# Kernel optimization log

Measured on AMD Instinct MI355X. Metric: run time of the kernel, lower is better.

Reference implementation:

```python
import jax, jax.numpy as jnp
import numpy as np

GROUP_SIZE = 128
TOP_K = 2
ZERO_POINT = 8  # Marlin symmetric zero point: w = scale * (q - 8)


def _dequant_int4(q, scales, group_size):
    # q: [E, N, K] int values in [0,15]; scales: [E, N, K//group_size]
    s = jnp.repeat(scales, group_size, axis=-1)  # [E, N, K]
    return (q.astype(jnp.float32) - float(ZERO_POINT)) * s


def setup_inputs() -> dict:
    key = jax.random.key(0)
    k1, k2, k3, k4, k5, k6 = jax.random.split(key, 6)
    B, S, H, I, E = 2, 1024, 2048, 1408, 8
    router_logits = jax.random.normal(k1, (B, S, E), dtype=jnp.float32)
    hidden_states = jax.random.normal(k2, (B, S, H), dtype=jnp.float32)
    fc_gate_up_qweights = jax.random.randint(k3, (E, 2 * I, H), 0, 16, dtype=jnp.int32)
    fc_gate_up_scales = jax.random.uniform(k4, (E, 2 * I, H // GROUP_SIZE), dtype=jnp.float32) * 0.02
    fc_down_qweights = jax.random.randint(k5, (E, H, I), 0, 16, dtype=jnp.int32)
    fc_down_scales = jax.random.uniform(k6, (E, H, I // GROUP_SIZE), dtype=jnp.float32) * 0.02
    return {
        "router_logits": router_logits,
        "hidden_states": hidden_states,
        "fc_gate_up_qweights": fc_gate_up_qweights,
        "fc_gate_up_scales": fc_gate_up_scales,
        "fc_down_qweights": fc_down_qweights,
        "fc_down_scales": fc_down_scales,
    }


def reference(router_logits, hidden_states, fc_gate_up_qweights, fc_gate_up_scales,
              fc_down_qweights, fc_down_scales):
    B, S, H = hidden_states.shape
    E = router_logits.shape[-1]
    T = B * S
    x = hidden_states.reshape(T, H)
    logits = router_logits.reshape(T, E)

    # top-k routing with softmax over selected logits
    top_vals, top_idx = jax.lax.top_k(logits, TOP_K)          # [T, k]
    top_w = jax.nn.softmax(top_vals, axis=-1)                 # [T, k]
    route_w = jnp.zeros((T, E), x.dtype).at[jnp.arange(T)[:, None], top_idx].set(top_w)  # [T, E]

    # dequantize int4 weights: scale * (q - 8), per-group along K
    w_gate_up = _dequant_int4(fc_gate_up_qweights, fc_gate_up_scales, GROUP_SIZE)  # [E, 2I, H]
    w_down = _dequant_int4(fc_down_qweights, fc_down_scales, GROUP_SIZE)          # [E, H, I]

    # grouped GEMM (dense over experts, masked by routing weights)
    gu = jnp.einsum('th,enh->ten', x, w_gate_up)              # [T, E, 2I]
    gate, up = jnp.split(gu, 2, axis=-1)
    act = jax.nn.silu(gate) * up                              # SwiGLU, [T, E, I]
    out = jnp.einsum('tei,ehi,te->th', act, w_down, route_w)  # [T, H]
    return out.reshape(B, S, H)
```

## Files before the change

kernel.cpp:

```cpp
#include <hip/hip_runtime.h>
#include <hip/hip_fp16.h>

#define T_TOKENS 2048
#define H_DIM    2048
#define I_DIM    1408
#define E_NUM    8

typedef _Float16 f16;
typedef __attribute__((ext_vector_type(8))) _Float16 f16x8;
typedef __attribute__((ext_vector_type(4))) float    floatx4;
typedef __attribute__((ext_vector_type(4))) unsigned uintx4;

static const size_t OFF_COUNTS = 0;
static const size_t OFF_LISTS  = 256;
static const size_t OFF_WLISTS = OFF_LISTS + (size_t)T_TOKENS * E_NUM * 4;
static const size_t OFF_XB     = 131328;
static const size_t OFF_ACT    = OFF_XB + (size_t)T_TOKENS * H_DIM * 2;
static const size_t OFF_GUPK   = OFF_ACT + (size_t)2 * T_TOKENS * I_DIM * 2;
static const size_t OFF_DNPK   = OFF_GUPK + (size_t)E_NUM * 22 * 32 * 128 * 8 * 4;
static const size_t OFF_TMP    = OFF_DNPK + (size_t)E_NUM * 16 * 22 * 128 * 8 * 4;


__global__ __launch_bounds__(256) void pack_gu_kernel(const int* __restrict__ q,
                                                      unsigned* __restrict__ out)
{
    const int b = blockIdx.x;
    const int g = threadIdx.x;
    const int4* qp = reinterpret_cast<const int4*>(q + (size_t)b * H_DIM) + g * 2;
    int4 a = qp[0], c = qp[1];
    unsigned d = (unsigned)(a.x & 15)        | ((unsigned)(a.z & 15) << 4)  |
                 ((unsigned)(c.x & 15) << 8) | ((unsigned)(c.z & 15) << 12) |
                 ((unsigned)(a.y & 15) << 16)| ((unsigned)(a.w & 15) << 20) |
                 ((unsigned)(c.y & 15) << 24)| ((unsigned)(c.w & 15) << 28);
    const int e = b / 2816;
    const int grow = b - e * 2816;
    const int is_up = grow >= I_DIM;
    const int icol  = grow - (is_up ? I_DIM : 0);
    const int nt    = icol >> 6;
    const int r     = ((((icol >> 4) & 3) * 2 + is_up) * 16) + (icol & 15);
    const int kt    = g >> 3, gg = g & 7;
    out[((((size_t)e * 22 + nt) * 32 + kt) * 128 + r) * 8 + (gg ^ (r & 7))] = d;
}

__global__ __launch_bounds__(256) void pack_dn_kernel(const int* __restrict__ q,
                                                      unsigned* __restrict__ out)
{
    const int b = blockIdx.x;
    const int t = threadIdx.x;
    if (t >= 176) return;
    const int4* qp = reinterpret_cast<const int4*>(q + (size_t)b * I_DIM) + t * 2;
    int4 a = qp[0], c = qp[1];
    unsigned d = (unsigned)(a.x & 15)        | ((unsigned)(a.z & 15) << 4)  |
                 ((unsigned)(c.x & 15) << 8) | ((unsigned)(c.z & 15) << 12) |
                 ((unsigned)(a.y & 15) << 16)| ((unsigned)(a.w & 15) << 20) |
                 ((unsigned)(c.y & 15) << 24)| ((unsigned)(c.w & 15) << 28);
    const int e = b >> 11;
    const int grow = b & 2047;
    const int nt = grow >> 7;
    const int r  = grow & 127;
    const int kt = t >> 3, gg = t & 7;
    out[((((size_t)e * 16 + nt) * 22 + kt) * 128 + r) * 8 + (gg ^ (r & 7))] = d;
}

__global__ void xconv_kernel(const float* __restrict__ x, f16* __restrict__ xb)
{
    int i = blockIdx.x * blockDim.x + threadIdx.x;
    const float4* x4 = reinterpret_cast<const float4*>(x) + (size_t)i * 2;
    float4 v0 = x4[0], v1 = x4[1];
    f16x8 bv;
    bv[0] = (f16)v0.x; bv[1] = (f16)v0.y; bv[2] = (f16)v0.z; bv[3] = (f16)v0.w;
    bv[4] = (f16)v1.x; bv[5] = (f16)v1.y; bv[6] = (f16)v1.z; bv[7] = (f16)v1.w;
    *reinterpret_cast<f16x8*>(xb + (size_t)i * 8) = bv;
}

__global__ void router_kernel(const float* __restrict__ logits,
                              int* __restrict__ counts,
                              int* __restrict__ lists,
                              float* __restrict__ wlists)
{
    int t = blockIdx.x * blockDim.x + threadIdx.x;
    if (t >= T_TOKENS) return;
    const float* l = logits + (size_t)t * E_NUM;
    float v0 = -1e30f, v1 = -1e30f;
    int i0 = 0, i1 = 0;
    #pragma unroll
    for (int e = 0; e < E_NUM; ++e) {
        float v = l[e];
        if (v > v0) { v1 = v0; i1 = i0; v0 = v; i0 = e; }
        else if (v > v1) { v1 = v; i1 = e; }
    }
    float w0 = 1.f / (1.f + __expf(v1 - v0));
    float w1 = 1.f - w0;
    int p0 = atomicAdd(&counts[i0], 1);
    lists[i0 * T_TOKENS + p0] = t * 2 + 0;
    wlists[i0 * T_TOKENS + p0] = w0;
    int p1 = atomicAdd(&counts[i1], 1);
    lists[i1 * T_TOKENS + p1] = t * 2 + 1;
    wlists[i1 * T_TOKENS + p1] = w1;
}

__device__ __forceinline__ f16x8 dq8(unsigned d, __half2 s2)
{
    const __half2 off = __floats2half2_rn(1032.f, 1032.f);
    unsigned t0 = (d         & 0x000F000Fu) | 0x64006400u;
    unsigned t1 = ((d >> 4)  & 0x000F000Fu) | 0x64006400u;
    unsigned t2 = ((d >> 8)  & 0x000F000Fu) | 0x64006400u;
    unsigned t3 = ((d >> 12) & 0x000F000Fu) | 0x64006400u;
    uintx4 w;
    w.x = __builtin_bit_cast(unsigned, __hmul2(__hsub2(__builtin_bit_cast(__half2, t0), off), s2));
    w.y = __builtin_bit_cast(unsigned, __hmul2(__hsub2(__builtin_bit_cast(__half2, t1), off), s2));
    w.z = __builtin_bit_cast(unsigned, __hmul2(__hsub2(__builtin_bit_cast(__half2, t2), off), s2));
    w.w = __builtin_bit_cast(unsigned, __hmul2(__hsub2(__builtin_bit_cast(__half2, t3), off), s2));
    return __builtin_bit_cast(f16x8, w);
}

__global__ __launch_bounds__(256) void gemm1_kernel(
    const f16*      __restrict__ xb,
    const unsigned* __restrict__ qpk,
    const float*    __restrict__ sc,
    const int*      __restrict__ counts,
    const int*      __restrict__ lists,
    f16*            __restrict__ act)
{
    const int e   = blockIdx.z;
    const int cnt = counts[e];
    const int m0  = blockIdx.y * 128;
    if (m0 >= cnt) return;
    const int nt  = blockIdx.x;

    __shared__ __align__(16) f16 Al[8192];
    __shared__ unsigned Blu[1024];
    __shared__ float scl[128 * 17];
    __shared__ int meta[128];

    const int tid = threadIdx.x;
    if (tid < 128) {
        int m = m0 + tid;
        meta[tid] = lists[e * T_TOKENS + (m < cnt ? m : 0)];
    }
    for (int i = tid; i < 2048; i += 256) {
        int r = i >> 4, grp = i & 15;
        int tt = r >> 4, within = r & 15;
        int grow = ((tt & 1) ? I_DIM : 0) + nt * 64 + (tt >> 1) * 16 + within;
        scl[r * 17 + grp] = sc[(size_t)(e * 2816 + grow) * 16 + grp];
    }
    __syncthreads();

    const int lane = tid & 63;
    const int wv = tid >> 6;
    const int wm = wv >> 1, wn = wv & 1;

    int    aoff[4];
    size_t agbl[4];
    #pragma unroll
    for (int j = 0; j < 4; ++j) {
        int g = tid + 256 * j;
        int arow = g >> 3, cg = g & 7;
        aoff[j] = arow * 64 + ((cg ^ (arow & 7)) * 8);
        agbl[j] = (size_t)(meta[arow] >> 1) * H_DIM + cg * 8;
    }
    const unsigned* bt = qpk + ((size_t)e * 22 + nt) * (32 * 1024);

    floatx4 acc[4][4];
    #pragma unroll
    for (int i = 0; i < 4; ++i)
        #pragma unroll
        for (int j = 0; j < 4; ++j)
            acc[i][j] = (floatx4){0.f, 0.f, 0.f, 0.f};

    for (int kt = 0; kt < 32; ++kt) {
        #pragma unroll
        for (int j = 0; j < 4; ++j) {
            f16x8 v = *reinterpret_cast<const f16x8*>(xb + agbl[j] + kt * 64);
            *reinterpret_cast<f16x8*>(&Al[aoff[j]]) = v;
        }
        const unsigned* bsrc = bt + kt * 1024;
        #pragma unroll
        for (int j = 0; j < 4; ++j)
            Blu[tid + j * 256] = bsrc[tid + j * 256];
        __syncthreads();

        const int grp = kt >> 1;
        #pragma unroll
        for (int ks = 0; ks < 2; ++ks) {
            const int gidx = ks * 4 + (lane >> 4);
            f16x8 af[4], bf[4];
            #pragma unroll
            for (int mt = 0; mt < 4; ++mt) {
                int ra = wm * 64 + mt * 16 + (lane & 15);
                af[mt] = *reinterpret_cast<const f16x8*>(&Al[ra * 64 + ((gidx ^ (ra & 7)) * 8)]);
            }
            #pragma unroll
            for (int ntf = 0; ntf < 4; ++ntf) {
                int rb = wn * 64 + ntf * 16 + (lane & 15);
                __half2 s2 = __float2half2_rn(scl[rb * 17 + grp]);
                unsigned d = Blu[rb * 8 + (gidx ^ (rb & 7))];
                bf[ntf] = dq8(d, s2);
            }
            #pragma unroll
            for (int mt = 0; mt < 4; ++mt)
                #pragma unroll
                for (int ntf = 0; ntf < 4; ++ntf)
                    acc[mt][ntf] = __builtin_amdgcn_mfma_f32_16x16x32_f16(af[mt], bf[ntf], acc[mt][ntf], 0, 0, 0);
        }
        __syncthreads();
    }

    const int rbase = (lane >> 4) * 4;
    const int cn = lane & 15;
    #pragma unroll
    for (int mt = 0; mt < 4; ++mt) {
        #pragma unroll
        for (int j = 0; j < 2; ++j) {
            floatx4 g = acc[mt][2 * j];
            floatx4 u = acc[mt][2 * j + 1];
            int col = nt * 64 + (wn * 2 + j) * 16 + cn;
            #pragma unroll
            for (int r = 0; r < 4; ++r) {
                int lrow = wm * 64 + mt * 16 + rbase + r;
                if (m0 + lrow < cnt) {
                    float gate = g[r], up = u[r];
                    float a = gate / (1.f + __expf(-gate)) * up;
                    act[(size_t)meta[lrow] * I_DIM + col] = (f16)a;
                }
            }
        }
    }
}

__global__ __launch_bounds__(256) void gemm2_kernel(
    const f16*      __restrict__ act,
    const unsigned* __restrict__ qpk,
    const float*    __restrict__ sc,
    const int*      __restrict__ counts,
    const int*      __restrict__ lists,
    const float*    __restrict__ wlists,
    float*          __restrict__ tmp)
{
    const int e   = blockIdx.z;
    const int cnt = counts[e];
    const int m0  = blockIdx.y * 128;
    if (m0 >= cnt) return;
    const int nt  = blockIdx.x;

    __shared__ __align__(16) f16 Al[8192];
    __shared__ unsigned Blu[1024];
    __shared__ float scl[128 * 12];
    __shared__ int   meta[128];
    __shared__ float wmeta[128];

    const int tid = threadIdx.x;
    if (tid < 128) {
        int m = m0 + tid;
        int mm = (m < cnt) ? m : 0;
        meta[tid]  = lists[e * T_TOKENS + mm];
        wmeta[tid] = wlists[e * T_TOKENS + mm];
    }
    for (int i = tid; i < 1408; i += 256) {
        int r = i / 11, grp = i - r * 11;
        scl[r * 12 + grp] = sc[(size_t)(e * 2048 + nt * 128 + r) * 11 + grp];
    }
    __syncthreads();

    const int lane = tid & 63;
    const int wv = tid >> 6;
    const int wm = wv >> 1, wn = wv & 1;

    int    aoff[4];
    size_t agbl[4];
    #pragma unroll
    for (int j = 0; j < 4; ++j) {
        int g = tid + 256 * j;
        int arow = g >> 3, cg = g & 7;
        aoff[j] = arow * 64 + ((cg ^ (arow & 7)) * 8);
        agbl[j] = (size_t)meta[arow] * I_DIM + cg * 8;
    }
    const unsigned* bt = qpk + ((size_t)e * 16 + nt) * (22 * 1024);

    floatx4 acc[4][4];
    #pragma unroll
    for (int i = 0; i < 4; ++i)
        #pragma unroll
        for (int j = 0; j < 4; ++j)
            acc[i][j] = (floatx4){0.f, 0.f, 0.f, 0.f};

    for (int kt = 0; kt < 22; ++kt) {
        #pragma unroll
        for (int j = 0; j < 4; ++j) {
            f16x8 v = *reinterpret_cast<const f16x8*>(act + agbl[j] + kt * 64);
            *reinterpret_cast<f16x8*>(&Al[aoff[j]]) = v;
        }
        const unsigned* bsrc = bt + kt * 1024;
        #pragma unroll
        for (int j = 0; j < 4; ++j)
            Blu[tid + j * 256] = bsrc[tid + j * 256];
        __syncthreads();

        const int grp = kt >> 1;
        #pragma unroll
        for (int ks = 0; ks < 2; ++ks) {
            const int gidx = ks * 4 + (lane >> 4);
            f16x8 af[4], bf[4];
            #pragma unroll
            for (int mt = 0; mt < 4; ++mt) {
                int ra = wm * 64 + mt * 16 + (lane & 15);
                af[mt] = *reinterpret_cast<const f16x8*>(&Al[ra * 64 + ((gidx ^ (ra & 7)) * 8)]);
            }
            #pragma unroll
            for (int ntf = 0; ntf < 4; ++ntf) {
                int rb = wn * 64 + ntf * 16 + (lane & 15);
                __half2 s2 = __float2half2_rn(scl[rb * 12 + grp]);
                unsigned d = Blu[rb * 8 + (gidx ^ (rb & 7))];
                bf[ntf] = dq8(d, s2);
            }
            #pragma unroll
            for (int mt = 0; mt < 4; ++mt)
                #pragma unroll
                for (int ntf = 0; ntf < 4; ++ntf)
                    acc[mt][ntf] = __builtin_amdgcn_mfma_f32_16x16x32_f16(af[mt], bf[ntf], acc[mt][ntf], 0, 0, 0);
        }
        __syncthreads();
    }

    const int rbase = (lane >> 4) * 4;
    const int cn = lane & 15;
    #pragma unroll
    for (int mt = 0; mt < 4; ++mt) {
        #pragma unroll
        for (int ntf = 0; ntf < 4; ++ntf) {
            floatx4 v = acc[mt][ntf];
            int col = nt * 128 + wn * 64 + ntf * 16 + cn;
            #pragma unroll
            for (int r = 0; r < 4; ++r) {
                int lrow = wm * 64 + mt * 16 + rbase + r;
                if (m0 + lrow < cnt) {
                    tmp[(size_t)meta[lrow] * H_DIM + col] = wmeta[lrow] * v[r];
                }
            }
        }
    }
}

__global__ void finalize_kernel(const float* __restrict__ tmp, float* __restrict__ out)
{
    int i4 = blockIdx.x * blockDim.x + threadIdx.x;
    int t  = i4 >> 9;
    int h  = (i4 & 511) * 4;
    float4 a = *reinterpret_cast<const float4*>(tmp + ((size_t)2 * t) * H_DIM + h);
    float4 b = *reinterpret_cast<const float4*>(tmp + ((size_t)(2 * t + 1)) * H_DIM + h);
    float4 o;
    o.x = a.x + b.x; o.y = a.y + b.y; o.z = a.z + b.z; o.w = a.w + b.w;
    *reinterpret_cast<float4*>(out + (size_t)t * H_DIM + h) = o;
}

extern "C" void kernel_launch(void* const* d_in, const int* in_sizes, int n_in,
                              void* d_out, int out_size, void* d_ws, size_t ws_size,
                              hipStream_t stream)
{
    const float* router_logits = (const float*)d_in[0];
    const float* x             = (const float*)d_in[1];
    const int*   gu_q          = (const int*)d_in[2];
    const float* gu_s          = (const float*)d_in[3];
    const int*   dn_q          = (const int*)d_in[4];
    const float* dn_s          = (const float*)d_in[5];
    float* out = (float*)d_out;

    char* ws = (char*)d_ws;
    int*      counts = (int*)(ws + OFF_COUNTS);
    int*      lists  = (int*)(ws + OFF_LISTS);
    float*    wlists = (float*)(ws + OFF_WLISTS);
    f16*      xb     = (f16*)(ws + OFF_XB);
    f16*      act    = (f16*)(ws + OFF_ACT);
    unsigned* gu_pk  = (unsigned*)(ws + OFF_GUPK);
    unsigned* dn_pk  = (unsigned*)(ws + OFF_DNPK);
    float*    tmp    = (float*)(ws + OFF_TMP);

    hipMemsetAsync(counts, 0, E_NUM * sizeof(int), stream);

    pack_gu_kernel<<<E_NUM * 2816, 256, 0, stream>>>(gu_q, gu_pk);
    pack_dn_kernel<<<E_NUM * 2048, 256, 0, stream>>>(dn_q, dn_pk);
    xconv_kernel<<<T_TOKENS * H_DIM / 8 / 256, 256, 0, stream>>>(x, xb);
    router_kernel<<<T_TOKENS / 256, 256, 0, stream>>>(router_logits, counts, lists, wlists);

    gemm1_kernel<<<dim3(22, 16, 8), 256, 0, stream>>>(xb, gu_pk, gu_s, counts, lists, act);
    gemm2_kernel<<<dim3(16, 16, 8), 256, 0, stream>>>(act, dn_pk, dn_s, counts, lists, wlists, tmp);
    finalize_kernel<<<4096, 256, 0, stream>>>(tmp, out);
}
```

Before: 561.1 us.

## Double-buffer LDS tiles in both MoE GEMMs and halve gemm2 N-tile

Both grouped GEMM kernels now keep two LDS buffers. They prefetch the next K-tile from global memory into registers while the current tile feeds the MFMAs, which leaves one barrier per iteration instead of two. Scale conversions are hoisted out of the inner ks loop. gemm2's N tile shrinks from 128 to 64, and the weight packing layout and grid change to match, doubling the block count to fill the GPU better at the cost of more activation reloads and more LDS per block.

```diff
diff --git a/kernel.cpp b/kernel.cpp
--- a/kernel.cpp
+++ b/kernel.cpp
@@ -18,7 +18,7 @@
 static const size_t OFF_ACT    = OFF_XB + (size_t)T_TOKENS * H_DIM * 2;
 static const size_t OFF_GUPK   = OFF_ACT + (size_t)2 * T_TOKENS * I_DIM * 2;
 static const size_t OFF_DNPK   = OFF_GUPK + (size_t)E_NUM * 22 * 32 * 128 * 8 * 4;
-static const size_t OFF_TMP    = OFF_DNPK + (size_t)E_NUM * 16 * 22 * 128 * 8 * 4;
+static const size_t OFF_TMP    = OFF_DNPK + (size_t)E_NUM * 32 * 22 * 64 * 8 * 4;
 
 
 __global__ __launch_bounds__(256) void pack_gu_kernel(const int* __restrict__ q,
@@ -56,10 +56,10 @@
                  ((unsigned)(c.y & 15) << 24)| ((unsigned)(c.w & 15) << 28);
     const int e = b >> 11;
     const int grow = b & 2047;
-    const int nt = grow >> 7;
-    const int r  = grow & 127;
+    const int nt = grow >> 6;
+    const int r  = grow & 63;
     const int kt = t >> 3, gg = t & 7;
-    out[((((size_t)e * 16 + nt) * 22 + kt) * 128 + r) * 8 + (gg ^ (r & 7))] = d;
+    out[((((size_t)e * 32 + nt) * 22 + kt) * 64 + r) * 8 + (gg ^ (r & 7))] = d;
 }
 
 __global__ void xconv_kernel(const float* __restrict__ x, f16* __restrict__ xb)
@@ -128,8 +128,8 @@
     if (m0 >= cnt) return;
     const int nt  = blockIdx.x;
 
-    __shared__ __align__(16) f16 Al[8192];
-    __shared__ unsigned Blu[1024];
+    __shared__ __align__(16) f16 Al[2][8192];
+    __shared__ unsigned Blu[2][1024];
     __shared__ float scl[128 * 17];
     __shared__ int meta[128];
 
@@ -140,8 +140,8 @@
     }
     for (int i = tid; i < 2048; i += 256) {
         int r = i >> 4, grp = i & 15;
-        int tt = r >> 4, within = r & 15;
-        int grow = ((tt & 1) ? I_DIM : 0) + nt * 64 + (tt >> 1) * 16 + within;
+        int tt = r >> 4;
+        int grow = ((tt & 1) ? I_DIM : 0) + nt * 64 + (tt >> 1) * 16 + (r & 15);
         scl[r * 17 + grp] = sc[(size_t)(e * 2816 + grow) * 16 + grp];
     }
     __syncthreads();
@@ -168,19 +168,34 @@
         for (int j = 0; j < 4; ++j)
             acc[i][j] = (floatx4){0.f, 0.f, 0.f, 0.f};
 
+    f16x8    areg[4];
+    unsigned breg[4];
+    #pragma unroll
+    for (int j = 0; j < 4; ++j) areg[j] = *reinterpret_cast<const f16x8*>(xb + agbl[j]);
+    #pragma unroll
+    for (int j = 0; j < 4; ++j) breg[j] = bt[tid + j * 256];
+    #pragma unroll
+    for (int j = 0; j < 4; ++j) *reinterpret_cast<f16x8*>(&Al[0][aoff[j]]) = areg[j];
+    #pragma unroll
+    for (int j = 0; j < 4; ++j) Blu[0][tid + j * 256] = breg[j];
+    __syncthreads();
+
     for (int kt = 0; kt < 32; ++kt) {
-        #pragma unroll
-        for (int j = 0; j < 4; ++j) {
-            f16x8 v = *reinterpret_cast<const f16x8*>(xb + agbl[j] + kt * 64);
-            *reinterpret_cast<f16x8*>(&Al[aoff[j]]) = v;
-        }
-        const unsigned* bsrc = bt + kt * 1024;
-        #pragma unroll
-        for (int j = 0; j < 4; ++j)
-            Blu[tid + j * 256] = bsrc[tid + j * 256];
-        __syncthreads();
-
+        const int cur = kt & 1;
+        if (kt < 31) {
+            #pragma unroll
+            for (int j = 0; j < 4; ++j)
+                areg[j] = *reinterpret_cast<const f16x8*>(xb + agbl[j] + (kt + 1) * 64);
+            #pragma unroll
+            for (int j = 0; j < 4; ++j)
+                breg[j] = bt[(kt + 1) * 1024 + tid + j * 256];
+        }
         const int grp = kt >> 1;
+        __half2 s2v[4];
+        #pragma unroll
+        for (int ntf = 0; ntf < 4; ++ntf)
+            s2v[ntf] = __float2half2_rn(scl[(wn * 64 + ntf * 16 + (lane & 15)) * 17 + grp]);
+
         #pragma unroll
         for (int ks = 0; ks < 2; ++ks) {
             const int gidx = ks * 4 + (lane >> 4);
@@ -188,20 +203,24 @@
             #pragma unroll
             for (int mt = 0; mt < 4; ++mt) {
                 int ra = wm * 64 + mt * 16 + (lane & 15);
-                af[mt] = *reinterpret_cast<const f16x8*>(&Al[ra * 64 + ((gidx ^ (ra & 7)) * 8)]);
+                af[mt] = *reinterpret_cast<const f16x8*>(&Al[cur][ra * 64 + ((gidx ^ (ra & 7)) * 8)]);
             }
             #pragma unroll
             for (int ntf = 0; ntf < 4; ++ntf) {
                 int rb = wn * 64 + ntf * 16 + (lane & 15);
-                __half2 s2 = __float2half2_rn(scl[rb * 17 + grp]);
-                unsigned d = Blu[rb * 8 + (gidx ^ (rb & 7))];
-                bf[ntf] = dq8(d, s2);
+                bf[ntf] = dq8(Blu[cur][rb * 8 + (gidx ^ (rb & 7))], s2v[ntf]);
             }
             #pragma unroll
             for (int mt = 0; mt < 4; ++mt)
                 #pragma unroll
                 for (int ntf = 0; ntf < 4; ++ntf)
                     acc[mt][ntf] = __builtin_amdgcn_mfma_f32_16x16x32_f16(af[mt], bf[ntf], acc[mt][ntf], 0, 0, 0);
+        }
+        if (kt < 31) {
+            #pragma unroll
+            for (int j = 0; j < 4; ++j) *reinterpret_cast<f16x8*>(&Al[cur ^ 1][aoff[j]]) = areg[j];
+            #pragma unroll
+            for (int j = 0; j < 4; ++j) Blu[cur ^ 1][tid + j * 256] = breg[j];
         }
         __syncthreads();
     }
@@ -243,9 +262,9 @@
     if (m0 >= cnt) return;
     const int nt  = blockIdx.x;
 
-    __shared__ __align__(16) f16 Al[8192];
-    __shared__ unsigned Blu[1024];
-    __shared__ float scl[128 * 12];
+    __shared__ __align__(16) f16 Al[2][8192];
+    __shared__ unsigned Blu[2][512];
+    __shared__ float scl[64 * 12];
     __shared__ int   meta[128];
     __shared__ float wmeta[128];
 
@@ -256,9 +275,9 @@
         meta[tid]  = lists[e * T_TOKENS + mm];
         wmeta[tid] = wlists[e * T_TOKENS + mm];
     }
-    for (int i = tid; i < 1408; i += 256) {
+    for (int i = tid; i < 704; i += 256) {
         int r = i / 11, grp = i - r * 11;
-        scl[r * 12 + grp] = sc[(size_t)(e * 2048 + nt * 128 + r) * 11 + grp];
+        scl[r * 12 + grp] = sc[(size_t)(e * 2048 + nt * 64 + r) * 11 + grp];
     }
     __syncthreads();
 
@@ -275,49 +294,68 @@
         aoff[j] = arow * 64 + ((cg ^ (arow & 7)) * 8);
         agbl[j] = (size_t)meta[arow] * I_DIM + cg * 8;
     }
-    const unsigned* bt = qpk + ((size_t)e * 16 + nt) * (22 * 1024);
-
-    floatx4 acc[4][4];
+    const unsigned* bt = qpk + ((size_t)e * 32 + nt) * (22 * 512);
+
+    floatx4 acc[4][2];
     #pragma unroll
     for (int i = 0; i < 4; ++i)
         #pragma unroll
-        for (int j = 0; j < 4; ++j)
+        for (int j = 0; j < 2; ++j)
             acc[i][j] = (floatx4){0.f, 0.f, 0.f, 0.f};
 
+    f16x8    areg[4];
+    unsigned breg[2];
+    #pragma unroll
+    for (int j = 0; j < 4; ++j) areg[j] = *reinterpret_cast<const f16x8*>(act + agbl[j]);
+    #pragma unroll
+    for (int j = 0; j < 2; ++j) breg[j] = bt[tid + j * 256];
+    #pragma unroll
+    for (int j = 0; j < 4; ++j) *reinterpret_cast<f16x8*>(&Al[0][aoff[j]]) = areg[j];
+    #pragma unroll
+    for (int j = 0; j < 2; ++j) Blu[0][tid + j * 256] = breg[j];
+    __syncthreads();
+
     for (int kt = 0; kt < 22; ++kt) {
-        #pragma unroll
-        for (int j = 0; j < 4; ++j) {
-            f16x8 v = *reinterpret_cast<const f16x8*>(act + agbl[j] + kt * 64);
-            *reinterpret_cast<f16x8*>(&Al[aoff[j]]) = v;
-        }
-        const unsigned* bsrc = bt + kt * 1024;
-        #pragma unroll
-        for (int j = 0; j < 4; ++j)
-            Blu[tid + j * 256] = bsrc[tid + j * 256];
-        __syncthreads();
-
+        const int cur = kt & 1;
+        if (kt < 21) {
+            #pragma unroll
+            for (int j = 0; j < 4; ++j)
+                areg[j] = *reinterpret_cast<const f16x8*>(act + agbl[j] + (kt + 1) * 64);
+            #pragma unroll
+            for (int j = 0; j < 2; ++j)
+                breg[j] = bt[(kt + 1) * 512 + tid + j * 256];
+        }
         const int grp = kt >> 1;
+        __half2 s2v[2];
+        #pragma unroll
+        for (int ntf = 0; ntf < 2; ++ntf)
+            s2v[ntf] = __float2half2_rn(scl[(wn * 32 + ntf * 16 + (lane & 15)) * 12 + grp]);
+
         #pragma unroll
         for (int ks = 0; ks < 2; ++ks) {
             const int gidx = ks * 4 + (lane >> 4);
-            f16x8 af[4], bf[4];
+            f16x8 af[4], bf[2];
             #pragma unroll
             for (int mt = 0; mt < 4; ++mt) {
                 int ra = wm * 64 + mt * 16 + (lane & 15);
-                af[mt] = *reinterpret_cast<const f16x8*>(&Al[ra * 64 + ((gidx ^ (ra & 7)) * 8)]);
-            }
-            #pragma unroll
-            for (int ntf = 0; ntf < 4; ++ntf) {
-                int rb = wn * 64 + ntf * 16 + (lane & 15);
-                __half2 s2 = __float2half2_rn(scl[rb * 12 + grp]);
-                unsigned d = Blu[rb * 8 + (gidx ^ (rb & 7))];
-                bf[ntf] = dq8(d, s2);
+                af[mt] = *reinterpret_cast<const f16x8*>(&Al[cur][ra * 64 + ((gidx ^ (ra & 7)) * 8)]);
+            }
+            #pragma unroll
+            for (int ntf = 0; ntf < 2; ++ntf) {
+                int rb = wn * 32 + ntf * 16 + (lane & 15);
+                bf[ntf] = dq8(Blu[cur][rb * 8 + (gidx ^ (rb & 7))], s2v[ntf]);
             }
             #pragma unroll
             for (int mt = 0; mt < 4; ++mt)
                 #pragma unroll
-                for (int ntf = 0; ntf < 4; ++ntf)
+                for (int ntf = 0; ntf < 2; ++ntf)
                     acc[mt][ntf] = __builtin_amdgcn_mfma_f32_16x16x32_f16(af[mt], bf[ntf], acc[mt][ntf], 0, 0, 0);
+        }
+        if (kt < 21) {
+            #pragma unroll
+            for (int j = 0; j < 4; ++j) *reinterpret_cast<f16x8*>(&Al[cur ^ 1][aoff[j]]) = areg[j];
+            #pragma unroll
+            for (int j = 0; j < 2; ++j) Blu[cur ^ 1][tid + j * 256] = breg[j];
         }
         __syncthreads();
     }
@@ -327,9 +365,9 @@
     #pragma unroll
     for (int mt = 0; mt < 4; ++mt) {
         #pragma unroll
-        for (int ntf = 0; ntf < 4; ++ntf) {
+        for (int ntf = 0; ntf < 2; ++ntf) {
             floatx4 v = acc[mt][ntf];
-            int col = nt * 128 + wn * 64 + ntf * 16 + cn;
+            int col = nt * 64 + wn * 32 + ntf * 16 + cn;
             #pragma unroll
             for (int r = 0; r < 4; ++r) {
                 int lrow = wm * 64 + mt * 16 + rbase + r;
@@ -383,6 +421,6 @@
     router_kernel<<<T_TOKENS / 256, 256, 0, stream>>>(router_logits, counts, lists, wlists);
 
     gemm1_kernel<<<dim3(22, 16, 8), 256, 0, stream>>>(xb, gu_pk, gu_s, counts, lists, act);
-    gemm2_kernel<<<dim3(16, 16, 8), 256, 0, stream>>>(act, dn_pk, dn_s, counts, lists, wlists, tmp);
+    gemm2_kernel<<<dim3(32, 16, 8), 256, 0, stream>>>(act, dn_pk, dn_s, counts, lists, wlists, tmp);
     finalize_kernel<<<4096, 256, 0, stream>>>(tmp, out);
 }
```

Result: faster. 537.7 us (-4.2%).
